# Kernel tuning notes

Hardware: AMD Instinct MI355X
Metric: run time of the kernel (lower is better)

Reference implementation:

```python
import jax, jax.numpy as jnp
import numpy as np

B, S, D = 2, 4096, 1024
H, DK, DV = 4, 128, 256          # head_k_dim, head_v_dim
KD, VD = H * DK, H * DV          # key_dim=512, value_dim=1024
RANK = 16                        # gate_low_rank_dim
GLN = 16.0                       # gate_logit_normalizer
EPS = 1e-5
C = 64                           # chunk size
NC = S // C


def setup_inputs() -> dict:
    key = jax.random.key(0)
    ks = jax.random.split(key, 9)
    w = lambda k, shape: (jax.random.normal(k, shape, jnp.float32) * 0.02)
    return {
        "x": jax.random.normal(ks[0], (B, S, D), jnp.float32),
        "Wq": w(ks[1], (D, KD)),
        "Wk": w(ks[2], (D, KD)),
        "Wv": w(ks[3], (D, VD)),
        "Wgk1": w(ks[4], (D, RANK)),
        "Wgk2": w(ks[5], (RANK, KD)),
        "bgk": jnp.zeros((KD,), jnp.float32),
        "Wg": w(ks[6], (D, VD)),
        "Wo": w(ks[7], (VD, D)),
        "norm_w": jnp.ones((DV,), jnp.float32),
    }


def _gla_chunk(q, k, v, gk):
    """Chunkwise gated linear attention. q,k,gk: [B,S,H,DK]; v: [B,S,H,DV]."""
    qc = q.reshape(B, NC, C, H, DK)
    kc = k.reshape(B, NC, C, H, DK)
    vc = v.reshape(B, NC, C, H, DV)
    gc = gk.reshape(B, NC, C, H, DK)
    gcum = jnp.cumsum(gc, axis=2)                       # inclusive within-chunk cumsum (<= 0)
    g_last = gcum[:, :, -1]                             # [B,NC,H,DK]
    q_t = qc * jnp.exp(gcum)                            # q decayed forward
    k_inv = kc * jnp.exp(-gcum)                         # for intra-chunk scores
    k_dec = kc * jnp.exp(g_last[:, :, None] - gcum)     # for state update (bounded)
    # intra-chunk causal scores
    A = jnp.einsum('bnthk,bnshk->bnhts', q_t, k_inv)    # [B,NC,H,C,C]
    mask = jnp.tril(jnp.ones((C, C), bool))
    A = jnp.where(mask, A, 0.0)
    o_intra = jnp.einsum('bnhts,bnshv->bnthv', A, vc)   # [B,NC,C,H,DV]
    # per-chunk state contribution
    kv = jnp.einsum('bnthk,bnthv->bnhkv', k_dec, vc)    # [B,NC,H,DK,DV]

    def step(state, inp):
        q_tc, gl, kvc = inp                             # [B,C,H,DK], [B,H,DK], [B,H,DK,DV]
        o_inter = jnp.einsum('bthk,bhkv->bthv', q_tc, state)
        state = state * jnp.exp(gl)[..., None] + kvc
        return state, o_inter

    xs = (jnp.swapaxes(q_t, 0, 1), jnp.swapaxes(g_last, 0, 1), jnp.swapaxes(kv, 0, 1))
    init = jnp.zeros((B, H, DK, DV), q.dtype)
    _, o_inter = jax.lax.scan(step, init, xs)           # [NC,B,C,H,DV]
    o = o_intra + jnp.swapaxes(o_inter, 0, 1)
    return o.reshape(B, S, H, DV)


def reference(x, Wq, Wk, Wv, Wgk1, Wgk2, bgk, Wg, Wo, norm_w):
    scale = DK ** -0.5
    q = (x @ Wq).reshape(B, S, H, DK) * scale
    k = (x @ Wk).reshape(B, S, H, DK)
    v = (x @ Wv).reshape(B, S, H, DV)
    gk = (jax.nn.log_sigmoid((x @ Wgk1) @ Wgk2 + bgk) / GLN).reshape(B, S, H, DK)
    o = _gla_chunk(q, k, v, gk)                          # [B,S,H,DV]
    # fused RMSNorm + swish gate (per-head norm over DV)
    g = (x @ Wg).reshape(B, S, H, DV)
    o = o * jax.lax.rsqrt(jnp.mean(o * o, axis=-1, keepdims=True) + EPS) * norm_w
    o = o * (g * jax.nn.sigmoid(g))
    return o.reshape(B, S, VD) @ Wo
```

## Files before the change

kernel.cpp:

```cpp
#include <hip/hip_runtime.h>

typedef __bf16 bf16_t;
typedef __bf16 bf16x8 __attribute__((ext_vector_type(8)));
typedef float  f32x4  __attribute__((ext_vector_type(4)));

#define MFMA16(a,b,c) __builtin_amdgcn_mfma_f32_16x16x32_bf16((a),(b),(c),0,0,0)

#define SCALE_Q 0.08838834764831845f

#define GLOBAL_LOAD_LDS16(gptr, lptr)                                          \
  __builtin_amdgcn_global_load_lds(                                            \
      (const __attribute__((address_space(1))) void*)(gptr),                   \
      (__attribute__((address_space(3))) void*)(lptr), 16, 0, 0)

__global__ __launch_bounds__(256) void k_convert(const void* __restrict__ src,
                                                 const unsigned int* __restrict__ nwp,
                                                 bf16_t* __restrict__ dst, int n) {
  bool isf32 = (nwp[0] == 0x3F800000u);
  int g = blockIdx.x * 256 + threadIdx.x;
  int i = g * 8;
  if (i >= n) return;
  if (isf32) {
    const float4* s = (const float4*)src;
    float4 a = s[g * 2], b = s[g * 2 + 1];
    bf16x8 o;
    o[0] = (bf16_t)a.x; o[1] = (bf16_t)a.y; o[2] = (bf16_t)a.z; o[3] = (bf16_t)a.w;
    o[4] = (bf16_t)b.x; o[5] = (bf16_t)b.y; o[6] = (bf16_t)b.z; o[7] = (bf16_t)b.w;
    *(bf16x8*)(dst + i) = o;
  } else {
    *(bf16x8*)(dst + i) = ((const bf16x8*)src)[g];
  }
}

__global__ __launch_bounds__(256) void k_convT(const void* __restrict__ src,
                                               const unsigned int* __restrict__ nwp,
                                               bf16_t* __restrict__ dst,
                                               int R, int Ccols) {
  __shared__ bf16_t t[32][33];
  bool isf32 = (nwp[0] == 0x3F800000u);
  int tx = threadIdx.x & 31, ty = threadIdx.x >> 5;
  int r0 = blockIdx.y * 32, c0 = blockIdx.x * 32;
#pragma unroll
  for (int i = 0; i < 4; i++) {
    int r = r0 + ty + i * 8, cc = c0 + tx;
    float v = isf32 ? ((const float*)src)[(size_t)r * Ccols + cc]
                    : (float)((const bf16_t*)src)[(size_t)r * Ccols + cc];
    t[ty + i * 8][tx] = (bf16_t)v;
  }
  __syncthreads();
#pragma unroll
  for (int i = 0; i < 4; i++) {
    int cc = c0 + ty + i * 8;
    dst[(size_t)cc * R + r0 + tx] = t[tx][ty + i * 8];
  }
}

__global__ __launch_bounds__(256) void k_gk1(const bf16_t* __restrict__ x,
                                             const bf16_t* __restrict__ W1,
                                             float* __restrict__ tmp) {
  int wave = threadIdx.x >> 6, lane = threadIdx.x & 63;
  int m = blockIdx.x * 4 + wave;
  const bf16_t* xr = x + (size_t)m * 1024;
  float p[16];
#pragma unroll
  for (int n = 0; n < 16; n++) p[n] = 0.f;
  for (int kk = 0; kk < 16; kk++) {
    int k = kk * 64 + lane;
    float xv = (float)xr[k];
    bf16x8 w0 = *(const bf16x8*)(W1 + k * 16);
    bf16x8 w1 = *(const bf16x8*)(W1 + k * 16 + 8);
#pragma unroll
    for (int j = 0; j < 8; j++) {
      p[j]     += xv * (float)w0[j];
      p[8 + j] += xv * (float)w1[j];
    }
  }
#pragma unroll
  for (int off = 1; off < 64; off <<= 1) {
#pragma unroll
    for (int n = 0; n < 16; n++) p[n] += __shfl_xor(p[n], off, 64);
  }
#pragma unroll
  for (int n = 0; n < 16; n++)
    if (lane == n) tmp[(size_t)m * 16 + n] = p[n];
}

__global__ __launch_bounds__(256) void k_gk2(const float* __restrict__ tmp,
                                             const bf16_t* __restrict__ W2,
                                             const bf16_t* __restrict__ bgk,
                                             float* __restrict__ gcum) {
  int g = blockIdx.x * 256 + threadIdx.x;
  int m = g >> 6;
  int n0 = (g & 63) * 8;
  float acc[8];
#pragma unroll
  for (int j = 0; j < 8; j++) acc[j] = 0.f;
  for (int k = 0; k < 16; k++) {
    float tv = tmp[(size_t)m * 16 + k];
    bf16x8 w = *(const bf16x8*)(W2 + k * 512 + n0);
#pragma unroll
    for (int j = 0; j < 8; j++) acc[j] += tv * (float)w[j];
  }
  int b = m >> 12, s = m & 4095;
  int h = n0 >> 7, dk0 = n0 & 127;
  float* dst = gcum + (((size_t)(b * 4 + h) * 4096 + s) * 128 + dk0);
#pragma unroll
  for (int j = 0; j < 8; j++) {
    float z = acc[j] + (float)bgk[n0 + j];
    float lg = -__logf(1.f + __expf(-z)) * (1.f / 16.f);
    dst[j] = fmaxf(lg, -4.0f);
  }
}

__global__ __launch_bounds__(128) void k_cumsum(float* __restrict__ gcum,
                                                float* __restrict__ glast) {
  int blk = blockIdx.x;
  int dk = threadIdx.x;
  float* base = gcum + (size_t)blk * 8192;
  float run = 0.f;
  for (int t = 0; t < 64; t++) {
    run += base[t * 128 + dk];
    base[t * 128 + dk] = run;
  }
  glast[(size_t)blk * 128 + dk] = run;
}

__global__ __launch_bounds__(256) void k_gemm(const bf16_t* __restrict__ Ag,
                                              const bf16_t* __restrict__ Bt,
                                              int mode,
                                              const float* __restrict__ gcum,
                                              const float* __restrict__ glast,
                                              bf16_t* __restrict__ qt,
                                              bf16_t* __restrict__ kinv,
                                              bf16_t* __restrict__ kdec,
                                              bf16_t* __restrict__ vr,
                                              bf16_t* __restrict__ gmat,
                                              float* __restrict__ fout) {
  __shared__ __attribute__((aligned(16))) bf16_t As[2 * 128 * 32];
  __shared__ __attribute__((aligned(16))) bf16_t Bs[2 * 128 * 32];
  int tid = threadIdx.x;
  int wave = tid >> 6, lane = tid & 63, quad = lane >> 4, c = lane & 15;
  int m0 = blockIdx.y * 128, n0 = blockIdx.x * 128;
  int wm = (wave >> 1) * 64, wn = (wave & 1) * 64;
  int r0s = wave * 32 + (lane >> 2);
  int r1s = r0s + 16;
  int s = lane & 3;
  int f0 = (s - (r0s >> 1)) & 3;
  int f1 = (s - (r1s >> 1)) & 3;
  const bf16_t* a0 = Ag + (size_t)(m0 + r0s) * 1024 + f0 * 8;
  const bf16_t* a1 = Ag + (size_t)(m0 + r1s) * 1024 + f1 * 8;
  const bf16_t* b0 = Bt + (size_t)(n0 + r0s) * 1024 + f0 * 8;
  const bf16_t* b1 = Bt + (size_t)(n0 + r1s) * 1024 + f1 * 8;
  bf16_t* lA = As + wave * 1024;
  bf16_t* lB = Bs + wave * 1024;
  int raOff[4], rbOff[4];
#pragma unroll
  for (int t4 = 0; t4 < 4; t4++) {
    int ra = wm + t4 * 16 + c;
    raOff[t4] = ra * 32 + (((quad + (ra >> 1)) & 3) * 8);
    int rb = wn + t4 * 16 + c;
    rbOff[t4] = rb * 32 + (((quad + (rb >> 1)) & 3) * 8);
  }
  GLOBAL_LOAD_LDS16(a0, lA);
  GLOBAL_LOAD_LDS16(a1, lA + 512);
  GLOBAL_LOAD_LDS16(b0, lB);
  GLOBAL_LOAD_LDS16(b1, lB + 512);
  f32x4 acc[4][4] = {};
  for (int k0 = 0; k0 < 1024; k0 += 32) {
    __syncthreads();
    int cur = (k0 >> 5) & 1;
    int nxtoff = (cur ^ 1) * 4096;
    if (k0 + 32 < 1024) {
      GLOBAL_LOAD_LDS16(a0 + k0 + 32, lA + nxtoff);
      GLOBAL_LOAD_LDS16(a1 + k0 + 32, lA + nxtoff + 512);
      GLOBAL_LOAD_LDS16(b0 + k0 + 32, lB + nxtoff);
      GLOBAL_LOAD_LDS16(b1 + k0 + 32, lB + nxtoff + 512);
    }
    int curoff = cur * 4096;
    bf16x8 af[4], bfr[4];
#pragma unroll
    for (int t4 = 0; t4 < 4; t4++) af[t4] = *(const bf16x8*)(As + curoff + raOff[t4]);
#pragma unroll
    for (int t4 = 0; t4 < 4; t4++) bfr[t4] = *(const bf16x8*)(Bs + curoff + rbOff[t4]);
#pragma unroll
    for (int mt = 0; mt < 4; mt++)
#pragma unroll
      for (int nt = 0; nt < 4; nt++)
        acc[mt][nt] = MFMA16(af[mt], bfr[nt], acc[mt][nt]);
  }
#pragma unroll
  for (int mt = 0; mt < 4; mt++)
#pragma unroll
    for (int nt = 0; nt < 4; nt++)
#pragma unroll
      for (int r = 0; r < 4; r++) {
        int m = m0 + wm + mt * 16 + quad * 4 + r;
        int n = n0 + wn + nt * 16 + c;
        float v = acc[mt][nt][r];
        if (mode == 1) {
          fout[(size_t)m * 1024 + n] = v;
        } else if (n0 < 512) {
          int b = m >> 12, ss = m & 4095, h = n >> 7, dk = n & 127;
          size_t idx = ((size_t)(b * 4 + h) * 4096 + ss) * 128 + dk;
          qt[idx] = (bf16_t)(v * SCALE_Q * __expf(gcum[idx]));
        } else if (n0 < 1024) {
          int nk = n - 512;
          int b = m >> 12, ss = m & 4095, h = nk >> 7, dk = nk & 127;
          size_t idx = ((size_t)(b * 4 + h) * 4096 + ss) * 128 + dk;
          float gc = gcum[idx];
          float gl = glast[((size_t)(b * 4 + h) * 64 + (ss >> 6)) * 128 + dk];
          kinv[idx] = (bf16_t)(v * __expf(fminf(-gc, 30.f)));
          kdec[idx] = (bf16_t)(v * __expf(gl - gc));
        } else if (n0 < 2048) {
          int nv = n - 1024;
          int b = m >> 12, ss = m & 4095, h = nv >> 8, dv = nv & 255;
          vr[((size_t)(b * 4 + h) * 4096 + ss) * 256 + dv] = (bf16_t)v;
        } else {
          gmat[(size_t)m * 1024 + (n - 2048)] = (bf16_t)v;
        }
      }
}

__global__ __launch_bounds__(256) void k_attA(const bf16_t* __restrict__ qt,
                                              const bf16_t* __restrict__ kinv,
                                              bf16_t* __restrict__ Aout) {
  int blk = blockIdx.x;
  size_t cb = (size_t)blk * 8192;
  int tid = threadIdx.x, wave = tid >> 6, lane = tid & 63;
  int quad = lane >> 4, c = lane & 15;
  f32x4 acc[4] = {};
  for (int kk = 0; kk < 128; kk += 32) {
    bf16x8 a = *(const bf16x8*)(qt + cb + (size_t)(wave * 16 + c) * 128 + kk + quad * 8);
#pragma unroll
    for (int nt = 0; nt < 4; nt++) {
      bf16x8 bb = *(const bf16x8*)(kinv + cb + (size_t)(nt * 16 + c) * 128 + kk + quad * 8);
      acc[nt] = MFMA16(a, bb, acc[nt]);
    }
  }
#pragma unroll
  for (int nt = 0; nt < 4; nt++)
#pragma unroll
    for (int r = 0; r < 4; r++) {
      int row = wave * 16 + quad * 4 + r, col = nt * 16 + c;
      Aout[(size_t)blk * 4096 + row * 64 + col] =
          (bf16_t)(col <= row ? acc[nt][r] : 0.f);
    }
}

__global__ __launch_bounds__(256) void k_kv(const bf16_t* __restrict__ kdec,
                                            const bf16_t* __restrict__ vr,
                                            bf16_t* __restrict__ kv) {
  int blk = blockIdx.x;
  __shared__ __attribute__((aligned(16))) bf16_t ls_kd[64 * 128];
  __shared__ __attribute__((aligned(16))) bf16_t ls_v[64 * 256];
  int tid = threadIdx.x, wave = tid >> 6, lane = tid & 63;
  int quad = lane >> 4, c = lane & 15;
  size_t cb = (size_t)blk * 8192;
  size_t cv = (size_t)blk * 16384;
  size_t sb = (size_t)blk * 32768;
#pragma unroll
  for (int j = 0; j < 4; j++) {
    int idx = tid + j * 256;
    int row = idx >> 4, col = (idx & 15) * 8;
    *(bf16x8*)&ls_kd[row * 128 + col] = *(const bf16x8*)(kdec + cb + (size_t)row * 128 + col);
  }
#pragma unroll
  for (int j = 0; j < 8; j++) {
    int idx = tid + j * 256;
    int row = idx >> 5, col = (idx & 31) * 8;
    *(bf16x8*)&ls_v[row * 256 + col] = *(const bf16x8*)(vr + cv + (size_t)row * 256 + col);
  }
  __syncthreads();
  int kbase = (wave >> 1) * 64;
  for (int pos = 0; pos < 2; pos++) {
    int dvbase = (wave & 1) * 64 + pos * 128;
    f32x4 acc[4][4] = {};
    for (int kk = 0; kk < 64; kk += 32) {
      bf16x8 a[4], bb[4];
#pragma unroll
      for (int mt = 0; mt < 4; mt++)
#pragma unroll
        for (int j = 0; j < 8; j++)
          a[mt][j] = ls_kd[(kk + quad * 8 + j) * 128 + kbase + mt * 16 + c];
#pragma unroll
      for (int nt = 0; nt < 4; nt++)
#pragma unroll
        for (int j = 0; j < 8; j++)
          bb[nt][j] = ls_v[(kk + quad * 8 + j) * 256 + dvbase + nt * 16 + c];
#pragma unroll
      for (int mt = 0; mt < 4; mt++)
#pragma unroll
        for (int nt = 0; nt < 4; nt++)
          acc[mt][nt] = MFMA16(a[mt], bb[nt], acc[mt][nt]);
    }
#pragma unroll
    for (int mt = 0; mt < 4; mt++)
#pragma unroll
      for (int nt = 0; nt < 4; nt++)
#pragma unroll
        for (int r = 0; r < 4; r++) {
          int kg = kbase + mt * 16 + quad * 4 + r;
          int dg = dvbase + nt * 16 + c;
          kv[sb + (size_t)kg * 256 + dg] = (bf16_t)acc[mt][nt][r];
        }
  }
}

__global__ __launch_bounds__(256) void k_scan2(bf16_t* __restrict__ states,
                                               const float* __restrict__ glast) {
  int g = blockIdx.x * 256 + threadIdx.x;
  int bh = g >> 15;
  int idx = g & 32767;
  int kg = idx >> 8;
  bf16_t* p = states + (size_t)bh * 64 * 32768 + idx;
  const float* gl = glast + (size_t)bh * 64 * 128 + kg;
  float carry = 0.f;
#pragma unroll 4
  for (int n = 0; n < 64; n++) {
    float kvv = (float)p[(size_t)n * 32768];
    float e = __expf(gl[n * 128]);
    p[(size_t)n * 32768] = (bf16_t)carry;
    carry = carry * e + kvv;
  }
}

__global__ __launch_bounds__(256) void k_o(const bf16_t* __restrict__ qt,
                                           const bf16_t* __restrict__ Amat,
                                           const bf16_t* __restrict__ vr,
                                           const bf16_t* __restrict__ states,
                                           const bf16_t* __restrict__ gmat,
                                           const bf16_t* __restrict__ normw,
                                           bf16_t* __restrict__ ob) {
  int blk = blockIdx.x;
  int bh = blk >> 6, n = blk & 63, b = bh >> 2, h = bh & 3;
  __shared__ __attribute__((aligned(16))) bf16_t ls[64 * 256];
  __shared__ __attribute__((aligned(16))) float lred[64][4];
  int tid = threadIdx.x, wave = tid >> 6, lane = tid & 63;
  int quad = lane >> 4, c = lane & 15;
  size_t cb = (size_t)blk * 8192;
  size_t cv = (size_t)blk * 16384;
  size_t sb = (size_t)blk * 32768;
  f32x4 acc[4][4] = {};
  for (int half = 0; half < 2; half++) {
    __syncthreads();
#pragma unroll
    for (int i = 0; i < 8; i++) {
      int idx = tid + i * 256;
      int row = idx >> 5, col = (idx & 31) * 8;
      *(bf16x8*)&ls[row * 256 + col] =
          *(const bf16x8*)(states + sb + (size_t)(half * 64 + row) * 256 + col);
    }
    __syncthreads();
    for (int kk2 = 0; kk2 < 2; kk2++) {
      int kl = kk2 * 32, kg = half * 64 + kl;
      bf16x8 a[4], bb[4];
#pragma unroll
      for (int mt = 0; mt < 4; mt++)
        a[mt] = *(const bf16x8*)(qt + cb + (size_t)(mt * 16 + c) * 128 + kg + quad * 8);
#pragma unroll
      for (int nt = 0; nt < 4; nt++)
#pragma unroll
        for (int j = 0; j < 8; j++)
          bb[nt][j] = ls[(kl + quad * 8 + j) * 256 + wave * 64 + nt * 16 + c];
#pragma unroll
      for (int mt = 0; mt < 4; mt++)
#pragma unroll
        for (int nt = 0; nt < 4; nt++)
          acc[mt][nt] = MFMA16(a[mt], bb[nt], acc[mt][nt]);
    }
  }
  __syncthreads();
#pragma unroll
  for (int i = 0; i < 8; i++) {
    int idx = tid + i * 256;
    int row = idx >> 5, col = (idx & 31) * 8;
    *(bf16x8*)&ls[row * 256 + col] =
        *(const bf16x8*)(vr + cv + (size_t)row * 256 + col);
  }
  __syncthreads();
  for (int kk = 0; kk < 64; kk += 32) {
    bf16x8 a[4], bb[4];
#pragma unroll
    for (int mt = 0; mt < 4; mt++)
      a[mt] = *(const bf16x8*)(Amat + (size_t)blk * 4096 + (size_t)(mt * 16 + c) * 64 + kk + quad * 8);
#pragma unroll
    for (int nt = 0; nt < 4; nt++)
#pragma unroll
      for (int j = 0; j < 8; j++)
        bb[nt][j] = ls[(kk + quad * 8 + j) * 256 + wave * 64 + nt * 16 + c];
#pragma unroll
    for (int mt = 0; mt < 4; mt++)
#pragma unroll
      for (int nt = 0; nt < 4; nt++)
        acc[mt][nt] = MFMA16(a[mt], bb[nt], acc[mt][nt]);
  }
  float p[4][4];
#pragma unroll
  for (int mt = 0; mt < 4; mt++)
#pragma unroll
    for (int r = 0; r < 4; r++) {
      float s = 0.f;
#pragma unroll
      for (int nt = 0; nt < 4; nt++) s += acc[mt][nt][r] * acc[mt][nt][r];
      p[mt][r] = s;
    }
#pragma unroll
  for (int off = 1; off < 16; off <<= 1) {
#pragma unroll
    for (int mt = 0; mt < 4; mt++)
#pragma unroll
      for (int r = 0; r < 4; r++) p[mt][r] += __shfl_xor(p[mt][r], off, 64);
  }
  if (c == 0) {
#pragma unroll
    for (int mt = 0; mt < 4; mt++)
#pragma unroll
      for (int r = 0; r < 4; r++) lred[mt * 16 + quad * 4 + r][wave] = p[mt][r];
  }
  __syncthreads();
#pragma unroll
  for (int mt = 0; mt < 4; mt++)
#pragma unroll
    for (int r = 0; r < 4; r++) {
      int row = mt * 16 + quad * 4 + r;
      float tot = lred[row][0] + lred[row][1] + lred[row][2] + lred[row][3];
      float rs = rsqrtf(tot * (1.f / 256.f) + 1e-5f);
      int sg = n * 64 + row;
      size_t gb = ((size_t)(b * 4096 + sg)) * 1024 + h * 256;
#pragma unroll
      for (int nt = 0; nt < 4; nt++) {
        int dv = wave * 64 + nt * 16 + c;
        float ov = acc[mt][nt][r] * rs * (float)normw[dv];
        float gv = (float)gmat[gb + dv];
        ov *= gv / (1.f + __expf(-gv));
        ob[gb + dv] = (bf16_t)ov;
      }
    }
}

extern "C" void kernel_launch(void* const* d_in, const int* in_sizes, int n_in,
                              void* d_out, int out_size, void* d_ws, size_t ws_size,
                              hipStream_t stream) {
  (void)in_sizes; (void)n_in; (void)out_size; (void)ws_size;
  const unsigned int* nw_oracle = (const unsigned int*)d_in[9];

  char* ws = (char*)d_ws;
  size_t off = 0;
  auto alloc = [&](size_t bytes) -> void* {
    void* p = ws + off;
    off += (bytes + 255) & ~(size_t)255;
    return p;
  };
  bf16_t* states = (bf16_t*)alloc((size_t)512 * 32768 * 2);
  bf16_t* cx     = states;
  float*  glast  = (float*) alloc((size_t)8 * 64 * 128 * 4);
  float*  tmp    = (float*) alloc((size_t)8192 * 16 * 4);
  float*  gcum   = (float*) alloc((size_t)8 * 4096 * 128 * 4);
  bf16_t* ob     = (bf16_t*)gcum;
  bf16_t* qt     = (bf16_t*)alloc((size_t)8 * 4096 * 128 * 2);
  bf16_t* kinv   = (bf16_t*)alloc((size_t)8 * 4096 * 128 * 2);
  bf16_t* kdec   = (bf16_t*)alloc((size_t)8 * 4096 * 128 * 2);
  bf16_t* vr     = (bf16_t*)alloc((size_t)8 * 4096 * 256 * 2);
  bf16_t* gmat   = (bf16_t*)alloc((size_t)8192 * 1024 * 2);
  bf16_t* Amat   = (bf16_t*)alloc((size_t)512 * 4096 * 2);
  bf16_t* tWcat  = (bf16_t*)alloc((size_t)3072 * 1024 * 2);
  bf16_t* cWgk1  = (bf16_t*)alloc((size_t)1024 * 16 * 2);
  bf16_t* cWgk2  = (bf16_t*)alloc((size_t)16 * 512 * 2);
  bf16_t* cbgk   = (bf16_t*)alloc((size_t)512 * 2);
  bf16_t* tWo    = (bf16_t*)alloc((size_t)1024 * 1024 * 2);
  bf16_t* cnw    = (bf16_t*)alloc((size_t)256 * 2);

  auto conv = [&](int i, bf16_t* dst, int n) {
    int blocks = (n + 2047) / 2048;
    k_convert<<<blocks, 256, 0, stream>>>(d_in[i], nw_oracle, dst, n);
  };
  auto convT = [&](int i, bf16_t* dst, int R, int Ccols) {
    k_convT<<<dim3(Ccols / 32, R / 32), 256, 0, stream>>>(d_in[i], nw_oracle, dst, R, Ccols);
  };
  conv(0, cx, 8192 * 1024);
  convT(1, tWcat, 1024, 512);
  convT(2, tWcat + (size_t)512 * 1024, 1024, 512);
  convT(3, tWcat + (size_t)1024 * 1024, 1024, 1024);
  conv(4, cWgk1, 1024 * 16);
  conv(5, cWgk2, 16 * 512);
  conv(6, cbgk, 512);
  convT(7, tWcat + (size_t)2048 * 1024, 1024, 1024);
  convT(8, tWo, 1024, 1024);
  conv(9, cnw, 256);

  k_gk1<<<2048, 256, 0, stream>>>(cx, cWgk1, tmp);
  k_gk2<<<2048, 256, 0, stream>>>(tmp, cWgk2, cbgk, gcum);
  k_cumsum<<<512, 128, 0, stream>>>(gcum, glast);
  k_gemm<<<dim3(24, 64), 256, 0, stream>>>(cx, tWcat, 0, gcum, glast,
                                           qt, kinv, kdec, vr, gmat, nullptr);
  k_attA<<<512, 256, 0, stream>>>(qt, kinv, Amat);
  k_kv<<<512, 256, 0, stream>>>(kdec, vr, states);
  k_scan2<<<1024, 256, 0, stream>>>(states, glast);
  k_o<<<512, 256, 0, stream>>>(qt, Amat, vr, states, gmat, cnw, ob);
  k_gemm<<<dim3(8, 64), 256, 0, stream>>>(ob, tWo, 1, nullptr, nullptr,
                                          nullptr, nullptr, nullptr, nullptr, nullptr,
                                          (float*)d_out);
}
```

Before: 361.5 us.

## Merge weight conversion launches into one kernel and add occupancy launch bounds

```diff
diff --git a/kernel.cpp b/kernel.cpp
--- a/kernel.cpp
+++ b/kernel.cpp
@@ -32,14 +32,14 @@
   }
 }
 
-__global__ __launch_bounds__(256) void k_convT(const void* __restrict__ src,
-                                               const unsigned int* __restrict__ nwp,
-                                               bf16_t* __restrict__ dst,
-                                               int R, int Ccols) {
-  __shared__ bf16_t t[32][33];
-  bool isf32 = (nwp[0] == 0x3F800000u);
+struct ConvSrcs {
+  const void *wq, *wk, *wv, *wg, *wo, *gk1, *gk2, *bgk, *nw;
+};
+__device__ __forceinline__ void convT_tile(const void* src, bf16_t* dst,
+                                           int Ccols, int bx, int by,
+                                           bool isf32, bf16_t (*t)[33]) {
   int tx = threadIdx.x & 31, ty = threadIdx.x >> 5;
-  int r0 = blockIdx.y * 32, c0 = blockIdx.x * 32;
+  int r0 = by * 32, c0 = bx * 32;
 #pragma unroll
   for (int i = 0; i < 4; i++) {
     int r = r0 + ty + i * 8, cc = c0 + tx;
@@ -51,7 +51,58 @@
 #pragma unroll
   for (int i = 0; i < 4; i++) {
     int cc = c0 + ty + i * 8;
-    dst[(size_t)cc * R + r0 + tx] = t[tx][ty + i * 8];
+    dst[(size_t)cc * 1024 + r0 + tx] = t[tx][ty + i * 8];
+  }
+}
+__device__ __forceinline__ void conv_straight(const void* src, bf16_t* dst,
+                                              int base_blk, int n, bool isf32) {
+  int g = (blockIdx.x - base_blk) * 256 + threadIdx.x;
+  int i = g * 8;
+  if (i >= n) return;
+  if (isf32) {
+    const float4* s = (const float4*)src;
+    float4 a = s[g * 2], b = s[g * 2 + 1];
+    bf16x8 o;
+    o[0] = (bf16_t)a.x; o[1] = (bf16_t)a.y; o[2] = (bf16_t)a.z; o[3] = (bf16_t)a.w;
+    o[4] = (bf16_t)b.x; o[5] = (bf16_t)b.y; o[6] = (bf16_t)b.z; o[7] = (bf16_t)b.w;
+    *(bf16x8*)(dst + i) = o;
+  } else {
+    *(bf16x8*)(dst + i) = ((const bf16x8*)src)[g];
+  }
+}
+__global__ __launch_bounds__(256) void k_convW(ConvSrcs s,
+                                               const unsigned int* __restrict__ nwp,
+                                               bf16_t* __restrict__ tWcat,
+                                               bf16_t* __restrict__ tWo,
+                                               bf16_t* __restrict__ cWgk1,
+                                               bf16_t* __restrict__ cWgk2,
+                                               bf16_t* __restrict__ cbgk,
+                                               bf16_t* __restrict__ cnw) {
+  __shared__ bf16_t t[32][33];
+  bool isf32 = (nwp[0] == 0x3F800000u);
+  int blk = blockIdx.x;
+  if (blk < 512) {
+    convT_tile(s.wq, tWcat, 512, blk & 15, blk >> 4, isf32, t);
+  } else if (blk < 1024) {
+    int b2 = blk - 512;
+    convT_tile(s.wk, tWcat + (size_t)512 * 1024, 512, b2 & 15, b2 >> 4, isf32, t);
+  } else if (blk < 2048) {
+    int b2 = blk - 1024;
+    convT_tile(s.wv, tWcat + (size_t)1024 * 1024, 1024, b2 & 31, b2 >> 5, isf32, t);
+  } else if (blk < 3072) {
+    int b2 = blk - 2048;
+    convT_tile(s.wg, tWcat + (size_t)2048 * 1024, 1024, b2 & 31, b2 >> 5, isf32, t);
+  } else if (blk < 4096) {
+    int b2 = blk - 3072;
+    convT_tile(s.wo, tWo, 1024, b2 & 31, b2 >> 5, isf32, t);
+  } else if (blk < 4104) {
+    conv_straight(s.gk1, cWgk1, 4096, 16384, isf32);
+  } else if (blk < 4108) {
+    conv_straight(s.gk2, cWgk2, 4104, 8192, isf32);
+  } else if (blk == 4108) {
+    conv_straight(s.bgk, cbgk, 4108, 512, isf32);
+  } else {
+    conv_straight(s.nw, cnw, 4109, 256, isf32);
   }
 }
 
@@ -125,7 +176,7 @@
   glast[(size_t)blk * 128 + dk] = run;
 }
 
-__global__ __launch_bounds__(256) void k_gemm(const bf16_t* __restrict__ Ag,
+__global__ __launch_bounds__(256, 4) void k_gemm(const bf16_t* __restrict__ Ag,
                                               const bf16_t* __restrict__ Bt,
                                               int mode,
                                               const float* __restrict__ gcum,
@@ -247,7 +298,7 @@
     }
 }
 
-__global__ __launch_bounds__(256) void k_kv(const bf16_t* __restrict__ kdec,
+__global__ __launch_bounds__(256, 3) void k_kv(const bf16_t* __restrict__ kdec,
                                             const bf16_t* __restrict__ vr,
                                             bf16_t* __restrict__ kv) {
   int blk = blockIdx.x;
@@ -324,7 +375,7 @@
   }
 }
 
-__global__ __launch_bounds__(256) void k_o(const bf16_t* __restrict__ qt,
+__global__ __launch_bounds__(256, 4) void k_o(const bf16_t* __restrict__ qt,
                                            const bf16_t* __restrict__ Amat,
                                            const bf16_t* __restrict__ vr,
                                            const bf16_t* __restrict__ states,
@@ -470,23 +521,11 @@
   bf16_t* tWo    = (bf16_t*)alloc((size_t)1024 * 1024 * 2);
   bf16_t* cnw    = (bf16_t*)alloc((size_t)256 * 2);
 
-  auto conv = [&](int i, bf16_t* dst, int n) {
-    int blocks = (n + 2047) / 2048;
-    k_convert<<<blocks, 256, 0, stream>>>(d_in[i], nw_oracle, dst, n);
-  };
-  auto convT = [&](int i, bf16_t* dst, int R, int Ccols) {
-    k_convT<<<dim3(Ccols / 32, R / 32), 256, 0, stream>>>(d_in[i], nw_oracle, dst, R, Ccols);
-  };
-  conv(0, cx, 8192 * 1024);
-  convT(1, tWcat, 1024, 512);
-  convT(2, tWcat + (size_t)512 * 1024, 1024, 512);
-  convT(3, tWcat + (size_t)1024 * 1024, 1024, 1024);
-  conv(4, cWgk1, 1024 * 16);
-  conv(5, cWgk2, 16 * 512);
-  conv(6, cbgk, 512);
-  convT(7, tWcat + (size_t)2048 * 1024, 1024, 1024);
-  convT(8, tWo, 1024, 1024);
-  conv(9, cnw, 256);
+  k_convert<<<4096, 256, 0, stream>>>(d_in[0], nw_oracle, cx, 8192 * 1024);
+  ConvSrcs cs{d_in[1], d_in[2], d_in[3], d_in[7], d_in[8],
+              d_in[4], d_in[5], d_in[6], d_in[9]};
+  k_convW<<<4110, 256, 0, stream>>>(cs, nw_oracle, tWcat, tWo,
+                                    cWgk1, cWgk2, cbgk, cnw);
 
   k_gk1<<<2048, 256, 0, stream>>>(cx, cWgk1, tmp);
   k_gk2<<<2048, 256, 0, stream>>>(tmp, cWgk2, cbgk, gcum);
```

New measurement: 345.4 us. 4.5% less time.
